# Performance work log

Measured on AMD Instinct MI355X. Metric: run time of the kernel, lower is better.

The kernel has to match this reference:

```python
import jax, jax.numpy as jnp
import numpy as np

N = 50000
E = 800000
IN_FEAT = 128
HEADS = 2
HEAD_DIM = 64  # hidden_feat // num_heads for 'concat'
HIDDEN = HEADS * HEAD_DIM
N_CLASSES = 16
NEG_SLOPE = 0.2
BN_EPS = 1e-5


def setup_inputs() -> dict:
    key = jax.random.key(0)
    ks = jax.random.split(key, 20)
    s = 0.1  # weight scale for numerical sanity
    return {
        "x": jax.random.normal(ks[0], (N, IN_FEAT), jnp.float32),
        "src0": jax.random.randint(ks[1], (E,), 0, N, jnp.int32),
        "dst0": jax.random.randint(ks[2], (E,), 0, N, jnp.int32),
        "ew0": jax.random.uniform(ks[3], (E,), jnp.float32),
        "src1": jax.random.randint(ks[4], (E,), 0, N, jnp.int32),
        "dst1": jax.random.randint(ks[5], (E,), 0, N, jnp.int32),
        "ew1": jax.random.uniform(ks[6], (E,), jnp.float32),
        "fc_w0": jax.random.normal(ks[7], (HIDDEN, IN_FEAT), jnp.float32) * s,
        "bias0": jnp.zeros((HIDDEN,), jnp.float32),
        "attn_l0": jax.random.normal(ks[8], (HEADS, HEAD_DIM), jnp.float32) * s,
        "attn_r0": jax.random.normal(ks[9], (HEADS, HEAD_DIM), jnp.float32) * s,
        "fc_w1": jax.random.normal(ks[10], (HIDDEN, IN_FEAT), jnp.float32) * s,
        "bias1": jnp.zeros((HIDDEN,), jnp.float32),
        "attn_l1": jax.random.normal(ks[11], (HEADS, HEAD_DIM), jnp.float32) * s,
        "attn_r1": jax.random.normal(ks[12], (HEADS, HEAD_DIM), jnp.float32) * s,
        "skip_w": jax.random.normal(ks[13], (HIDDEN, IN_FEAT), jnp.float32) * s,
        "skip_b": jnp.zeros((HIDDEN,), jnp.float32),
        "bn_gamma": jnp.ones((HIDDEN,), jnp.float32),
        "bn_beta": jnp.zeros((HIDDEN,), jnp.float32),
        "clf_w": jax.random.normal(ks[14], (N_CLASSES, HIDDEN), jnp.float32) * s,
        "clf_b": jnp.zeros((N_CLASSES,), jnp.float32),
    }


def _weighted_gat(x, src, dst, ew, fc_w, bias, attn_l, attn_r):
    # DGL GATConv with per-edge weight scaling of attention.
    f = (x @ fc_w.T).reshape(N, HEADS, HEAD_DIM)          # [N,H,D]
    el = jnp.sum(f * attn_l, axis=-1)                      # [N,H]
    er = jnp.sum(f * attn_r, axis=-1)                      # [N,H]
    e = jax.nn.leaky_relu(el[src] + er[dst], NEG_SLOPE)    # [E,H]
    # edge softmax over incoming edges of each dst, numerically stable
    m = jax.ops.segment_max(e, dst, num_segments=N)        # [N,H]
    ex = jnp.exp(e - m[dst])
    den = jax.ops.segment_sum(ex, dst, num_segments=N)     # [N,H]
    alpha = ex / den[dst]                                  # [E,H]
    alpha = alpha * ew[:, None]                            # edge-weight scaling
    msg = alpha[..., None] * f[src]                        # [E,H,D]
    out = jax.ops.segment_sum(msg, dst, num_segments=N)    # [N,H,D]
    return out + bias.reshape(1, HEADS, HEAD_DIM)


def reference(x, src0, dst0, ew0, src1, dst1, ew1,
              fc_w0, bias0, attn_l0, attn_r0,
              fc_w1, bias1, attn_l1, attn_r1,
              skip_w, skip_b, bn_gamma, bn_beta, clf_w, clf_b):
    # HeteroGraphConv with aggregate='sum': sum per-relation GAT outputs
    h2 = _weighted_gat(x, src0, dst0, ew0, fc_w0, bias0, attn_l0, attn_r0) \
       + _weighted_gat(x, src1, dst1, ew1, fc_w1, bias1, attn_l1, attn_r1)
    # multihead 'concat' aggregate with relu: flatten heads
    h2 = jax.nn.relu(h2).reshape(N, HIDDEN)
    # linear skip + residual add (dropout is identity at eval)
    h = (x @ skip_w.T + skip_b) + h2
    # classifier: BatchNorm1d (batch stats) -> ReLU -> Linear
    mu = jnp.mean(h, axis=0)
    var = jnp.mean((h - mu) ** 2, axis=0)
    hn = (h - mu) * jax.lax.rsqrt(var + BN_EPS) * bn_gamma + bn_beta
    logits = jax.nn.relu(hn) @ clf_w.T + clf_b
    return logits
```

## Files before the change

kernel.cpp:

```cpp
#include <hip/hip_runtime.h>
#include <hip/hip_bf16.h>

#define N_NODES 50000
#define N_EDGES 800000
#define HID 128
#define NEG_SLOPE 0.2f
#define BN_EPS 1e-5f

#define NBLK 256
#define BINSZ 512
#define BINSH 9
#define NBINS 98

typedef __bf16 v8bf __attribute__((ext_vector_type(8)));
typedef float v4f __attribute__((ext_vector_type(4)));

__device__ __forceinline__ float leaky(float v) {
    return (v > 0.f) ? v : v * NEG_SLOPE;
}
__device__ __forceinline__ unsigned int f2bu(float f) {
    __hip_bfloat16 b = __float2bfloat16(f);
    return (unsigned int)*reinterpret_cast<unsigned short*>(&b);
}
__device__ __forceinline__ unsigned int pack2bf(float lo, float hi) {
    return f2bu(lo) | (f2bu(hi) << 16);
}

__global__ __launch_bounds__(256) void k_prepw(const float* __restrict__ w0,
                                               const float* __restrict__ w1,
                                               const float* __restrict__ wsk,
                                               unsigned short* __restrict__ wb) {
    const int WQ = 128 * 128 / 4;
    int q = blockIdx.x * 256 + threadIdx.x;
    if (q >= 3 * WQ) return;
    int mat = q >> 12;
    int rem = q & 4095;
    const float* W = (mat == 0) ? w0 : (mat == 1) ? w1 : wsk;
    float4 v = ((const float4*)W)[rem];
    ushort4 o;
    o.x = (unsigned short)f2bu(v.x);
    o.y = (unsigned short)f2bu(v.y);
    o.z = (unsigned short)f2bu(v.z);
    o.w = (unsigned short)f2bu(v.w);
    *(ushort4*)(wb + (size_t)mat * 16384 + rem * 4) = o;
}

__global__ __launch_bounds__(256) void k_bincount(const int* __restrict__ dst0,
                                                  const int* __restrict__ dst1,
                                                  int* __restrict__ bincnt) {
    int rel = blockIdx.y;
    const int* dst = rel ? dst1 : dst0;
    __shared__ int cnt[NBINS];
    for (int i = threadIdx.x; i < NBINS; i += 256) cnt[i] = 0;
    __syncthreads();
    const int CH = (N_EDGES + NBLK - 1) / NBLK;
    int b0 = blockIdx.x * CH;
    int b1 = min(N_EDGES, b0 + CH);
    for (int e = b0 + threadIdx.x; e < b1; e += 256)
        atomicAdd(&cnt[dst[e] >> BINSH], 1);
    __syncthreads();
    for (int i = threadIdx.x; i < NBINS; i += 256)
        bincnt[rel * NBINS * NBLK + i * NBLK + blockIdx.x] = cnt[i];
}

__global__ __launch_bounds__(1024) void k_binscan(int* __restrict__ bincnt) {
    int* a = bincnt + blockIdx.x * NBINS * NBLK;
    const int TOT = NBINS * NBLK;
    const int CH = (TOT + 1023) / 1024;
    int tid = threadIdx.x;
    int base = tid * CH;
    int lv[CH];
    int sum = 0;
    for (int i = 0; i < CH; i++) {
        int idx = base + i;
        int v = (idx < TOT) ? a[idx] : 0;
        lv[i] = sum;
        sum += v;
    }
    __shared__ int ls[1024];
    ls[tid] = sum;
    __syncthreads();
    for (int ofs = 1; ofs < 1024; ofs <<= 1) {
        int v = (tid >= ofs) ? ls[tid - ofs] : 0;
        __syncthreads();
        ls[tid] += v;
        __syncthreads();
    }
    int pre = tid ? ls[tid - 1] : 0;
    for (int i = 0; i < CH; i++) {
        int idx = base + i;
        if (idx < TOT) a[idx] = pre + lv[i];
    }
}

__global__ __launch_bounds__(256) void k_binscatter(const int* __restrict__ dst0,
                                                    const int* __restrict__ dst1,
                                                    const int* __restrict__ src0,
                                                    const int* __restrict__ src1,
                                                    const float* __restrict__ ew0,
                                                    const float* __restrict__ ew1,
                                                    const int* __restrict__ bincnt,
                                                    int2* __restrict__ pairs0,
                                                    int2* __restrict__ pairs1) {
    int rel = blockIdx.y;
    const int* dst = rel ? dst1 : dst0;
    const int* src = rel ? src1 : src0;
    const float* ew = rel ? ew1 : ew0;
    int2* pairs = rel ? pairs1 : pairs0;
    __shared__ int cur[NBINS];
    for (int i = threadIdx.x; i < NBINS; i += 256)
        cur[i] = bincnt[rel * NBINS * NBLK + i * NBLK + blockIdx.x];
    __syncthreads();
    const int CH = (N_EDGES + NBLK - 1) / NBLK;
    int b0 = blockIdx.x * CH;
    int b1 = min(N_EDGES, b0 + CH);
    for (int e = b0 + threadIdx.x; e < b1; e += 256) {
        int d = dst[e];
        int pos = atomicAdd(&cur[d >> BINSH], 1);
        unsigned int packed = (unsigned int)(d & (BINSZ - 1)) |
                              ((unsigned int)src[e] << BINSH);
        pairs[pos] = make_int2((int)packed, __float_as_int(ew[e]));
    }
}

__global__ __launch_bounds__(256) void k_csr(const int* __restrict__ bincnt,
                                             const int2* __restrict__ pairs0,
                                             const int2* __restrict__ pairs1,
                                             const float* __restrict__ el0,
                                             const float* __restrict__ el1,
                                             int* __restrict__ offs0,
                                             int* __restrict__ offs1,
                                             int4* __restrict__ rec0,
                                             int4* __restrict__ rec1) {
    int rel = blockIdx.y;
    const int2* pairs = rel ? pairs1 : pairs0;
    const float* el = rel ? el1 : el0;
    int* offs = rel ? offs1 : offs0;
    int4* rec = rel ? rec1 : rec0;
    int bin = blockIdx.x;
    int tid = threadIdx.x;
    const int* bc = bincnt + rel * NBINS * NBLK;
    int pbase = bc[bin * NBLK];
    int pend = (bin < NBINS - 1) ? bc[(bin + 1) * NBLK] : N_EDGES;
    int n0 = bin << BINSH;
    int nn = min(N_NODES - n0, BINSZ);

    __shared__ int s_deg[BINSZ];
    __shared__ int s_ts[256];
    for (int i = tid; i < BINSZ; i += 256) s_deg[i] = 0;
    __syncthreads();
    for (int p = pbase + tid; p < pend; p += 256)
        atomicAdd(&s_deg[((unsigned int)pairs[p].x) & (BINSZ - 1)], 1);
    __syncthreads();

    int d0 = s_deg[tid * 2], d1 = s_deg[tid * 2 + 1];
    s_ts[tid] = d0 + d1;
    __syncthreads();
    for (int ofs = 1; ofs < 256; ofs <<= 1) {
        int v = (tid >= ofs) ? s_ts[tid - ofs] : 0;
        __syncthreads();
        s_ts[tid] += v;
        __syncthreads();
    }
    int pre = tid ? s_ts[tid - 1] : 0;
    s_deg[tid * 2] = pbase + pre;
    s_deg[tid * 2 + 1] = pbase + pre + d0;
    __syncthreads();

    for (int l = tid; l < nn; l += 256) offs[n0 + l] = s_deg[l];
    if (bin == NBINS - 1 && tid == 0) offs[N_NODES] = N_EDGES;
    __syncthreads();

    for (int p = pbase + tid; p < pend; p += 256) {
        int2 pr = pairs[p];
        unsigned int u = (unsigned int)pr.x;
        int dl = (int)(u & (BINSZ - 1));
        int s = (int)(u >> BINSH);
        int pos = atomicAdd(&s_deg[dl], 1);
        float2 ev = *(const float2*)(el + 2 * s);
        rec[pos] = make_int4(s, pr.y,
                             __float_as_int(ev.x), __float_as_int(ev.y));
    }
}

__global__ __launch_bounds__(256) void k_gemm_mfma(
    const float* __restrict__ x, const unsigned short* __restrict__ wb,
    const float* __restrict__ skip_b,
    const float* __restrict__ al0, const float* __restrict__ ar0,
    const float* __restrict__ al1, const float* __restrict__ ar1,
    unsigned short* __restrict__ fb0, unsigned short* __restrict__ fb1,
    float* __restrict__ el0, float* __restrict__ er0,
    float* __restrict__ el1, float* __restrict__ er1,
    float* __restrict__ hs) {
    __shared__ unsigned short As[64][128];
    int tid = threadIdx.x;
    int m0 = blockIdx.x * 64;

#pragma unroll
    for (int i = 0; i < 4; i++) {
        int idx = tid * 4 + i;
        int row = idx >> 4, seg = idx & 15;
        int gr = m0 + row;
        uint4 o = make_uint4(0, 0, 0, 0);
        if (gr < N_NODES) {
            const float* p = x + (size_t)gr * HID + seg * 8;
            float4 p0 = *(const float4*)p;
            float4 p1 = *(const float4*)(p + 4);
            o.x = pack2bf(p0.x, p0.y);
            o.y = pack2bf(p0.z, p0.w);
            o.z = pack2bf(p1.x, p1.y);
            o.w = pack2bf(p1.z, p1.w);
        }
        *(uint4*)(&As[row][(seg ^ (row & 7)) * 8]) = o;
    }
    __syncthreads();

    int w = tid >> 6, l = tid & 63;
    int lr = l & 15, lg = l >> 4;
    int arow = w * 16 + lr;
    v8bf afrag[4];
#pragma unroll
    for (int kb = 0; kb < 4; kb++)
        afrag[kb] = *(v8bf*)(&As[arow][((kb * 4 + lg) ^ (arow & 7)) * 8]);

    for (int s = 0; s < 6; s++) {
        int mat = s >> 1;
        int j0 = (s & 1) * 64;
        const unsigned short* wmat = wb + (size_t)mat * 16384;

        v4f acc[4] = {};
#pragma unroll
        for (int nt = 0; nt < 4; nt++) {
            const unsigned short* brow = wmat + (size_t)(j0 + nt * 16 + lr) * HID;
#pragma unroll
            for (int kb = 0; kb < 4; kb++) {
                v8bf bfrag = *(const v8bf*)(brow + kb * 32 + lg * 8);
                acc[nt] = __builtin_amdgcn_mfma_f32_16x16x32_bf16(
                    afrag[kb], bfrag, acc[nt], 0, 0, 0);
            }
        }

        if (mat < 2) {
            int h = s & 1;
            const float* al = mat ? al1 : al0;
            const float* ar = mat ? ar1 : ar0;
            float* elp = mat ? el1 : el0;
            float* erp = mat ? er1 : er0;
            unsigned short* fbp = mat ? fb1 : fb0;
            float elv[4] = {0.f, 0.f, 0.f, 0.f};
            float erv[4] = {0.f, 0.f, 0.f, 0.f};
#pragma unroll
            for (int nt = 0; nt < 4; nt++) {
                int colg = j0 + nt * 16 + lr;
                float av = al[colg], rv = ar[colg];
#pragma unroll
                for (int r = 0; r < 4; r++) {
                    elv[r] += acc[nt][r] * av;
                    erv[r] += acc[nt][r] * rv;
                }
            }
#pragma unroll
            for (int m = 1; m < 16; m <<= 1)
#pragma unroll
                for (int r = 0; r < 4; r++) {
                    elv[r] += __shfl_xor(elv[r], m);
                    erv[r] += __shfl_xor(erv[r], m);
                }
#pragma unroll
            for (int r = 0; r < 4; r++) {
                int grow = m0 + w * 16 + lg * 4 + r;
                if (grow >= N_NODES) continue;
#pragma unroll
                for (int nt = 0; nt < 4; nt++) {
                    int colg = j0 + nt * 16 + lr;
                    fbp[(size_t)grow * HID + colg] =
                        (unsigned short)f2bu(acc[nt][r]);
                }
                if (lr == 0) {
                    elp[grow * 2 + h] = elv[r];
                    erp[grow * 2 + h] = erv[r];
                }
            }
        } else {
#pragma unroll
            for (int r = 0; r < 4; r++) {
                int grow = m0 + w * 16 + lg * 4 + r;
                if (grow >= N_NODES) continue;
#pragma unroll
                for (int nt = 0; nt < 4; nt++) {
                    int colg = j0 + nt * 16 + lr;
                    hs[(size_t)grow * HID + colg] = acc[nt][r] + skip_b[colg];
                }
            }
        }
    }
}

__device__ __forceinline__ void agg_rel3(const int* __restrict__ offs,
                                         const int4* __restrict__ rec,
                                         const float* __restrict__ er,
                                         const unsigned short* __restrict__ fb,
                                         int n, int lane, int cb, int sub,
                                         int hh, float* a,
                                         unsigned long long* __restrict__ sed) {
    int b = offs[n];
    int e_end = offs[n + 1];
    int deg = e_end - b;
    if (deg <= 0) return;
    float ern0 = er[2 * n], ern1 = er[2 * n + 1];

    const int NC = 4;
    int cs[NC];
    float cw0[NC], cw1[NC];
    float d0 = 0.f, d1 = 0.f;
    int nchunk = (deg + 63) >> 6;
    for (int ch = 0; ch < nchunk; ch++) {
        int p = b + (ch << 6) + lane;
        int s = 0;
        float w0 = 0.f, w1 = 0.f;
        if (p < e_end) {
            int4 r = rec[p];
            s = r.x;
            float wgt = __int_as_float(r.y);
            float x0 = expf(leaky(__int_as_float(r.z) + ern0));
            float x1 = expf(leaky(__int_as_float(r.w) + ern1));
            d0 += x0;
            d1 += x1;
            w0 = x0 * wgt;
            w1 = x1 * wgt;
        }
        if (ch < NC) {
            cs[ch] = s;
            cw0[ch] = w0;
            cw1[ch] = w1;
        }
    }
#pragma unroll
    for (int m = 32; m; m >>= 1) {
        d0 += __shfl_xor(d0, m);
        d1 += __shfl_xor(d1, m);
    }
    float inv0 = 1.f / d0, inv1 = 1.f / d1;
    const unsigned short* fbc = fb + cb * 8;

    for (int ch = 0; ch < nchunk; ch++) {
        int s;
        unsigned int pk;
        if (ch < NC) {
            s = cs[ch];
            pk = pack2bf(cw0[ch] * inv0, cw1[ch] * inv1);
        } else {
            int p = b + (ch << 6) + lane;
            s = 0;
            pk = 0;
            if (p < e_end) {
                int4 r = rec[p];
                s = r.x;
                float wgt = __int_as_float(r.y);
                pk = pack2bf(expf(leaky(__int_as_float(r.z) + ern0)) * wgt * inv0,
                             expf(leaky(__int_as_float(r.w) + ern1)) * wgt * inv1);
            }
        }
        sed[lane] = ((unsigned long long)pk << 32) | (unsigned int)s;
        asm volatile("s_waitcnt lgkmcnt(0)" ::: "memory");
        int cnt = deg - (ch << 6);
        if (cnt > 64) cnt = 64;
        int ng = (cnt + 3) >> 2;
#pragma unroll 4
        for (int g = 0; g < ng; g++) {
            unsigned long long v = sed[(g << 2) + sub];
            int sj = (int)(unsigned int)v;
            unsigned int pkj = (unsigned int)(v >> 32);
            float aj = __uint_as_float(hh ? (pkj & 0xffff0000u) : (pkj << 16));
            uint4 fv = *(const uint4*)(fbc + (size_t)sj * HID);
            a[0] += aj * __uint_as_float(fv.x << 16);
            a[1] += aj * __uint_as_float(fv.x & 0xffff0000u);
            a[2] += aj * __uint_as_float(fv.y << 16);
            a[3] += aj * __uint_as_float(fv.y & 0xffff0000u);
            a[4] += aj * __uint_as_float(fv.z << 16);
            a[5] += aj * __uint_as_float(fv.z & 0xffff0000u);
            a[6] += aj * __uint_as_float(fv.w << 16);
            a[7] += aj * __uint_as_float(fv.w & 0xffff0000u);
        }
    }
}

__global__ __launch_bounds__(256) void k_aggregate(
    const int* __restrict__ offs0, const int4* __restrict__ rec0,
    const float* __restrict__ er0, const unsigned short* __restrict__ fb0,
    const int* __restrict__ offs1, const int4* __restrict__ rec1,
    const float* __restrict__ er1, const unsigned short* __restrict__ fb1,
    const float* __restrict__ bias0, const float* __restrict__ bias1,
    float* __restrict__ h) {
    __shared__ unsigned long long sed[4][64];
    int wave = threadIdx.x >> 6, lane = threadIdx.x & 63;
    int n = blockIdx.x * 4 + wave;
    if (n >= N_NODES) return;
    int cb = lane & 15;
    int sub = lane >> 4;
    int hh = cb >> 3;
    float a[8] = {0.f, 0.f, 0.f, 0.f, 0.f, 0.f, 0.f, 0.f};
    agg_rel3(offs0, rec0, er0, fb0, n, lane, cb, sub, hh, a, &sed[wave][0]);
    agg_rel3(offs1, rec1, er1, fb1, n, lane, cb, sub, hh, a, &sed[wave][0]);
#pragma unroll
    for (int j = 0; j < 8; j++) {
        a[j] += __shfl_xor(a[j], 16);
        a[j] += __shfl_xor(a[j], 32);
    }
    if (sub == 0) {
        size_t base = (size_t)n * HID + cb * 8;
        float4 v0 = *(const float4*)(h + base);
        float4 v1 = *(const float4*)(h + base + 4);
        int c0 = cb * 8;
        float4 o0, o1;
        o0.x = v0.x + fmaxf(a[0] + bias0[c0 + 0] + bias1[c0 + 0], 0.f);
        o0.y = v0.y + fmaxf(a[1] + bias0[c0 + 1] + bias1[c0 + 1], 0.f);
        o0.z = v0.z + fmaxf(a[2] + bias0[c0 + 2] + bias1[c0 + 2], 0.f);
        o0.w = v0.w + fmaxf(a[3] + bias0[c0 + 3] + bias1[c0 + 3], 0.f);
        o1.x = v1.x + fmaxf(a[4] + bias0[c0 + 4] + bias1[c0 + 4], 0.f);
        o1.y = v1.y + fmaxf(a[5] + bias0[c0 + 5] + bias1[c0 + 5], 0.f);
        o1.z = v1.z + fmaxf(a[6] + bias0[c0 + 6] + bias1[c0 + 6], 0.f);
        o1.w = v1.w + fmaxf(a[7] + bias0[c0 + 7] + bias1[c0 + 7], 0.f);
        *(float4*)(h + base) = o0;
        *(float4*)(h + base + 4) = o1;
    }
}

__global__ __launch_bounds__(256) void k_bnstats(const float* __restrict__ h,
                                                 double* __restrict__ psum,
                                                 double* __restrict__ psumsq) {
    int tid = threadIdx.x;
    const float4* h4 = (const float4*)h;
    double s[4] = {0.0, 0.0, 0.0, 0.0};
    double q[4] = {0.0, 0.0, 0.0, 0.0};
    const int totalv = N_NODES * HID / 4;
    const int stride = 512 * 256;
    for (int i = blockIdx.x * 256 + tid; i < totalv; i += stride) {
        float4 v = h4[i];
        s[0] += v.x; q[0] += (double)v.x * v.x;
        s[1] += v.y; q[1] += (double)v.y * v.y;
        s[2] += v.z; q[2] += (double)v.z * v.z;
        s[3] += v.w; q[3] += (double)v.w * v.w;
    }
    __shared__ double ls[256][4], lq[256][4];
#pragma unroll
    for (int j = 0; j < 4; j++) {
        ls[tid][j] = s[j];
        lq[tid][j] = q[j];
    }
    __syncthreads();
    if (tid < 32) {
#pragma unroll
        for (int j = 0; j < 4; j++) {
            double ss = 0.0, qq = 0.0;
            for (int t = tid; t < 256; t += 32) {
                ss += ls[t][j];
                qq += lq[t][j];
            }
            psum[blockIdx.x * 128 + tid * 4 + j] = ss;
            psumsq[blockIdx.x * 128 + tid * 4 + j] = qq;
        }
    }
}

__global__ void k_bn_finalize(const double* __restrict__ psum,
                              const double* __restrict__ psumsq,
                              const float* __restrict__ gamma,
                              const float* __restrict__ beta,
                              float* __restrict__ ss) {
    int c = threadIdx.x;
    double s = 0.0, q = 0.0;
    for (int b = 0; b < 512; b++) {
        s += psum[b * 128 + c];
        q += psumsq[b * 128 + c];
    }
    double mu = s / N_NODES;
    double var = q / N_NODES - mu * mu;
    float sc = gamma[c] * (float)(1.0 / sqrt(var + (double)BN_EPS));
    ss[c] = sc;
    ss[128 + c] = beta[c] - (float)mu * sc;
}

__global__ __launch_bounds__(256) void k_classify(const float* __restrict__ h,
                                                  const float* __restrict__ ss,
                                                  const float* __restrict__ clf_w,
                                                  const float* __restrict__ clf_b,
                                                  float* __restrict__ out) {
    int w = threadIdx.x >> 6, l = threadIdx.x & 63;
    int lr = l & 15, lg = l >> 4;
    int n0 = (blockIdx.x * 4 + w) * 16;
    if (n0 >= N_NODES) return;

    v8bf afrag[4], bfrag[4];
#pragma unroll
    for (int kb = 0; kb < 4; kb++) {
        int k0 = kb * 32 + lg * 8;
        const float* bp = clf_w + lr * HID + k0;
        float4 b0 = *(const float4*)bp;
        float4 b1 = *(const float4*)(bp + 4);
        bfrag[kb][0] = (__bf16)b0.x; bfrag[kb][1] = (__bf16)b0.y;
        bfrag[kb][2] = (__bf16)b0.z; bfrag[kb][3] = (__bf16)b0.w;
        bfrag[kb][4] = (__bf16)b1.x; bfrag[kb][5] = (__bf16)b1.y;
        bfrag[kb][6] = (__bf16)b1.z; bfrag[kb][7] = (__bf16)b1.w;
        const float* ap = h + (size_t)(n0 + lr) * HID + k0;
        float4 a0 = *(const float4*)ap;
        float4 a1 = *(const float4*)(ap + 4);
        float4 sc0 = *(const float4*)(ss + k0);
        float4 sc1 = *(const float4*)(ss + k0 + 4);
        float4 sh0 = *(const float4*)(ss + 128 + k0);
        float4 sh1 = *(const float4*)(ss + 128 + k0 + 4);
        afrag[kb][0] = (__bf16)fmaxf(a0.x * sc0.x + sh0.x, 0.f);
        afrag[kb][1] = (__bf16)fmaxf(a0.y * sc0.y + sh0.y, 0.f);
        afrag[kb][2] = (__bf16)fmaxf(a0.z * sc0.z + sh0.z, 0.f);
        afrag[kb][3] = (__bf16)fmaxf(a0.w * sc0.w + sh0.w, 0.f);
        afrag[kb][4] = (__bf16)fmaxf(a1.x * sc1.x + sh1.x, 0.f);
        afrag[kb][5] = (__bf16)fmaxf(a1.y * sc1.y + sh1.y, 0.f);
        afrag[kb][6] = (__bf16)fmaxf(a1.z * sc1.z + sh1.z, 0.f);
        afrag[kb][7] = (__bf16)fmaxf(a1.w * sc1.w + sh1.w, 0.f);
    }
    v4f acc = {};
#pragma unroll
    for (int kb = 0; kb < 4; kb++)
        acc = __builtin_amdgcn_mfma_f32_16x16x32_bf16(afrag[kb], bfrag[kb],
                                                      acc, 0, 0, 0);
    float cb = clf_b[lr];
#pragma unroll
    for (int r = 0; r < 4; r++) {
        int n = n0 + lg * 4 + r;
        out[(size_t)n * 16 + lr] = acc[r] + cb;
    }
}

extern "C" void kernel_launch(void* const* d_in, const int* in_sizes, int n_in,
                              void* d_out, int out_size, void* d_ws, size_t ws_size,
                              hipStream_t stream) {
    (void)in_sizes; (void)n_in; (void)out_size; (void)ws_size;
    const float* x      = (const float*)d_in[0];
    const int*   src0   = (const int*)d_in[1];
    const int*   dst0   = (const int*)d_in[2];
    const float* ew0    = (const float*)d_in[3];
    const int*   src1   = (const int*)d_in[4];
    const int*   dst1   = (const int*)d_in[5];
    const float* ew1    = (const float*)d_in[6];
    const float* fc_w0  = (const float*)d_in[7];
    const float* bias0  = (const float*)d_in[8];
    const float* al0    = (const float*)d_in[9];
    const float* ar0    = (const float*)d_in[10];
    const float* fc_w1  = (const float*)d_in[11];
    const float* bias1  = (const float*)d_in[12];
    const float* al1    = (const float*)d_in[13];
    const float* ar1    = (const float*)d_in[14];
    const float* skip_w = (const float*)d_in[15];
    const float* skip_b = (const float*)d_in[16];
    const float* gamma  = (const float*)d_in[17];
    const float* beta   = (const float*)d_in[18];
    const float* clf_w  = (const float*)d_in[19];
    const float* clf_b  = (const float*)d_in[20];
    float* out = (float*)d_out;

    char* wsp = (char*)d_ws;
    size_t off = 0;
    auto alloc = [&](size_t bytes) -> char* {
        char* p = wsp + off;
        off += (bytes + 255) & ~(size_t)255;
        return p;
    };
    unsigned short* wbf = (unsigned short*)alloc((size_t)3 * 16384 * 2);
    unsigned short* fb0 = (unsigned short*)alloc((size_t)N_NODES * HID * 2);
    unsigned short* fb1 = (unsigned short*)alloc((size_t)N_NODES * HID * 2);
    float*  hs     = (float*)alloc((size_t)N_NODES * HID * 4);
    float*  el0    = (float*)alloc((size_t)N_NODES * 2 * 4);
    float*  er0    = (float*)alloc((size_t)N_NODES * 2 * 4);
    float*  el1    = (float*)alloc((size_t)N_NODES * 2 * 4);
    float*  er1    = (float*)alloc((size_t)N_NODES * 2 * 4);
    int*    bincnt = (int*)alloc((size_t)2 * NBINS * NBLK * 4);
    int2*   pairs0 = (int2*)alloc((size_t)N_EDGES * 8);
    int2*   pairs1 = (int2*)alloc((size_t)N_EDGES * 8);
    int*    offs0  = (int*)alloc((size_t)(N_NODES + 1) * 4);
    int*    offs1  = (int*)alloc((size_t)(N_NODES + 1) * 4);
    int4*   rec0   = (int4*)alloc((size_t)N_EDGES * 16);
    int4*   rec1   = (int4*)alloc((size_t)N_EDGES * 16);
    double* psum   = (double*)alloc((size_t)512 * 128 * 8);
    double* psumsq = (double*)alloc((size_t)512 * 128 * 8);
    float*  ss     = (float*)alloc(256 * 4);

    k_prepw<<<48, 256, 0, stream>>>(fc_w0, fc_w1, skip_w, wbf);

    dim3 gbin(NBLK, 2);
    k_bincount<<<gbin, 256, 0, stream>>>(dst0, dst1, bincnt);
    k_binscan<<<2, 1024, 0, stream>>>(bincnt);
    k_binscatter<<<gbin, 256, 0, stream>>>(dst0, dst1, src0, src1, ew0, ew1,
                                           bincnt, pairs0, pairs1);

    k_gemm_mfma<<<(N_NODES + 63) / 64, 256, 0, stream>>>(
        x, wbf, skip_b, al0, ar0, al1, ar1,
        fb0, fb1, el0, er0, el1, er1, hs);

    dim3 gcsr(NBINS, 2);
    k_csr<<<gcsr, 256, 0, stream>>>(bincnt, pairs0, pairs1, el0, el1,
                                    offs0, offs1, rec0, rec1);

    k_aggregate<<<(N_NODES + 3) / 4, 256, 0, stream>>>(
        offs0, rec0, er0, fb0, offs1, rec1, er1, fb1, bias0, bias1, hs);

    k_bnstats<<<512, 256, 0, stream>>>(hs, psum, psumsq);
    k_bn_finalize<<<1, 128, 0, stream>>>(psum, psumsq, gamma, beta, ss);
    k_classify<<<(N_NODES + 63) / 64, 256, 0, stream>>>(
        hs, ss, clf_w, clf_b, out);
}
```

Before: 259.4 us.

## Stage weights in LDS for GEMM and use shuffles in aggregation

The GEMM now copies each 64x128 bf16 weight slice into swizzled shared memory before the MFMA loop, instead of reading B fragments straight from global memory. The aggregation kernel drops its LDS staging buffer and waitcnt, and broadcasts source index and packed attention weight across lanes with __shfl. Edge records now hold the source index pre-shifted to a byte offset, so the row address needs no multiply. Risks are extra __syncthreads in the GEMM, higher shuffle latency per gathered row, and the unroll dropping from 4 to 2.

```diff
diff --git a/kernel.cpp b/kernel.cpp
--- a/kernel.cpp
+++ b/kernel.cpp
@@ -178,7 +178,7 @@
         int s = (int)(u >> BINSH);
         int pos = atomicAdd(&s_deg[dl], 1);
         float2 ev = *(const float2*)(el + 2 * s);
-        rec[pos] = make_int4(s, pr.y,
+        rec[pos] = make_int4(s << 8, pr.y,
                              __float_as_int(ev.x), __float_as_int(ev.y));
     }
 }
@@ -193,6 +193,7 @@
     float* __restrict__ el1, float* __restrict__ er1,
     float* __restrict__ hs) {
     __shared__ unsigned short As[64][128];
+    __shared__ unsigned short Bs[64][128];
     int tid = threadIdx.x;
     int m0 = blockIdx.x * 64;
 
@@ -226,15 +227,25 @@
     for (int s = 0; s < 6; s++) {
         int mat = s >> 1;
         int j0 = (s & 1) * 64;
-        const unsigned short* wmat = wb + (size_t)mat * 16384;
+        const unsigned short* wmat = wb + (size_t)mat * 16384 + j0 * HID;
+        __syncthreads();
+#pragma unroll
+        for (int i = 0; i < 4; i++) {
+            int idx = tid * 4 + i;
+            int row = idx >> 4, seg = idx & 15;
+            uint4 wv = *(const uint4*)(wmat + row * HID + seg * 8);
+            *(uint4*)(&Bs[row][(seg ^ (row & 7)) * 8]) = wv;
+        }
+        __syncthreads();
 
         v4f acc[4] = {};
 #pragma unroll
         for (int nt = 0; nt < 4; nt++) {
-            const unsigned short* brow = wmat + (size_t)(j0 + nt * 16 + lr) * HID;
+            int brow = nt * 16 + lr;
 #pragma unroll
             for (int kb = 0; kb < 4; kb++) {
-                v8bf bfrag = *(const v8bf*)(brow + kb * 32 + lg * 8);
+                v8bf bfrag =
+                    *(v8bf*)(&Bs[brow][((kb * 4 + lg) ^ (brow & 7)) * 8]);
                 acc[nt] = __builtin_amdgcn_mfma_f32_16x16x32_bf16(
                     afrag[kb], bfrag, acc[nt], 0, 0, 0);
             }
@@ -296,13 +307,12 @@
     }
 }
 
-__device__ __forceinline__ void agg_rel3(const int* __restrict__ offs,
+__device__ __forceinline__ void agg_rel2(const int* __restrict__ offs,
                                          const int4* __restrict__ rec,
                                          const float* __restrict__ er,
-                                         const unsigned short* __restrict__ fb,
-                                         int n, int lane, int cb, int sub,
-                                         int hh, float* a,
-                                         unsigned long long* __restrict__ sed) {
+                                         const unsigned char* __restrict__ fbb,
+                                         int n, int lane, int sub,
+                                         int hh, float* a) {
     int b = offs[n];
     int e_end = offs[n + 1];
     int deg = e_end - b;
@@ -312,6 +322,7 @@
     const int NC = 4;
     int cs[NC];
     float cw0[NC], cw1[NC];
+    unsigned int cpk[NC];
     float d0 = 0.f, d1 = 0.f;
     int nchunk = (deg + 63) >> 6;
     for (int ch = 0; ch < nchunk; ch++) {
@@ -341,14 +352,16 @@
         d1 += __shfl_xor(d1, m);
     }
     float inv0 = 1.f / d0, inv1 = 1.f / d1;
-    const unsigned short* fbc = fb + cb * 8;
+#pragma unroll
+    for (int ch = 0; ch < NC; ch++)
+        cpk[ch] = pack2bf(cw0[ch] * inv0, cw1[ch] * inv1);
 
     for (int ch = 0; ch < nchunk; ch++) {
         int s;
         unsigned int pk;
         if (ch < NC) {
             s = cs[ch];
-            pk = pack2bf(cw0[ch] * inv0, cw1[ch] * inv1);
+            pk = cpk[ch];
         } else {
             int p = b + (ch << 6) + lane;
             s = 0;
@@ -357,22 +370,21 @@
                 int4 r = rec[p];
                 s = r.x;
                 float wgt = __int_as_float(r.y);
-                pk = pack2bf(expf(leaky(__int_as_float(r.z) + ern0)) * wgt * inv0,
-                             expf(leaky(__int_as_float(r.w) + ern1)) * wgt * inv1);
+                float w0 = expf(leaky(__int_as_float(r.z) + ern0)) * wgt;
+                float w1 = expf(leaky(__int_as_float(r.w) + ern1)) * wgt;
+                pk = pack2bf(w0 * inv0, w1 * inv1);
             }
         }
-        sed[lane] = ((unsigned long long)pk << 32) | (unsigned int)s;
-        asm volatile("s_waitcnt lgkmcnt(0)" ::: "memory");
         int cnt = deg - (ch << 6);
         if (cnt > 64) cnt = 64;
         int ng = (cnt + 3) >> 2;
-#pragma unroll 4
+#pragma unroll 2
         for (int g = 0; g < ng; g++) {
-            unsigned long long v = sed[(g << 2) + sub];
-            int sj = (int)(unsigned int)v;
-            unsigned int pkj = (unsigned int)(v >> 32);
+            int sl = (g << 2) + sub;
+            int sj = __shfl(s, sl);
+            unsigned int pkj = (unsigned int)__shfl((int)pk, sl);
             float aj = __uint_as_float(hh ? (pkj & 0xffff0000u) : (pkj << 16));
-            uint4 fv = *(const uint4*)(fbc + (size_t)sj * HID);
+            uint4 fv = *(const uint4*)(fbb + sj);
             a[0] += aj * __uint_as_float(fv.x << 16);
             a[1] += aj * __uint_as_float(fv.x & 0xffff0000u);
             a[2] += aj * __uint_as_float(fv.y << 16);
@@ -392,7 +404,6 @@
     const float* __restrict__ er1, const unsigned short* __restrict__ fb1,
     const float* __restrict__ bias0, const float* __restrict__ bias1,
     float* __restrict__ h) {
-    __shared__ unsigned long long sed[4][64];
     int wave = threadIdx.x >> 6, lane = threadIdx.x & 63;
     int n = blockIdx.x * 4 + wave;
     if (n >= N_NODES) return;
@@ -400,8 +411,10 @@
     int sub = lane >> 4;
     int hh = cb >> 3;
     float a[8] = {0.f, 0.f, 0.f, 0.f, 0.f, 0.f, 0.f, 0.f};
-    agg_rel3(offs0, rec0, er0, fb0, n, lane, cb, sub, hh, a, &sed[wave][0]);
-    agg_rel3(offs1, rec1, er1, fb1, n, lane, cb, sub, hh, a, &sed[wave][0]);
+    const unsigned char* fbb0 = (const unsigned char*)fb0 + cb * 16;
+    const unsigned char* fbb1 = (const unsigned char*)fb1 + cb * 16;
+    agg_rel2(offs0, rec0, er0, fbb0, n, lane, sub, hh, a);
+    agg_rel2(offs1, rec1, er1, fbb1, n, lane, sub, hh, a);
 #pragma unroll
     for (int j = 0; j < 8; j++) {
         a[j] += __shfl_xor(a[j], 16);
```

After: 221.4 us. 1.17x faster.
